# Kernel tuning notes

Hardware: AMD Instinct MI355X
Metric: run time of the kernel (lower is better)

Reference implementation:

```python
import jax, jax.numpy as jnp
import numpy as np

P = 30          # points per cloud (nr_points)
K = 20          # knn neighbors (k)
KS = 5          # spline kernel size (control points)
FN = 10         # filter_nr
EPS = 1e-8


def setup_inputs() -> dict:
    key = jax.random.key(0)
    ks = jax.random.split(key, 7)
    B = 16384
    pos = jax.random.normal(ks[0], (B * P, 3), dtype=jnp.float32)
    W = jax.random.normal(ks[1], (KS, FN), dtype=jnp.float32) * 0.5
    b_dsc = jnp.zeros((FN,), dtype=jnp.float32)
    w1 = jax.random.normal(ks[2], (FN, 256), dtype=jnp.float32) * (1.0 / np.sqrt(FN))
    b1 = jnp.zeros((256,), dtype=jnp.float32)
    w2 = jax.random.normal(ks[3], (256, 40), dtype=jnp.float32) * (1.0 / np.sqrt(256.0))
    b2 = jnp.zeros((40,), dtype=jnp.float32)
    return {"pos": pos, "W": W, "b_dsc": b_dsc, "w1": w1, "b1": b1, "w2": w2, "b2": b2}


def _dsc(pos, W, b_dsc):
    # pos: [N,3] -> per-point directional spline conv features [N, FN]
    B = pos.shape[0] // P
    p = pos.reshape(B, P, 3)
    # knn within each cloud (loop=False): pairwise sq dists, mask self
    d2 = jnp.sum((p[:, :, None, :] - p[:, None, :, :]) ** 2, axis=-1)  # [B,P,P]
    d2 = d2 + jnp.eye(P, dtype=d2.dtype) * 1e10
    _, idx = jax.lax.top_k(-d2, K)  # [B,P,K] nearest neighbor indices
    nb = jax.vmap(lambda pts, ii: pts[ii])(p, idx)  # [B,P,K,3] gather
    rel = nb - p[:, :, None, :]                      # [B,P,K,3]
    # normalize neighborhood into unit ball
    norm = jnp.sqrt(jnp.sum(rel * rel, axis=-1) + EPS)      # [B,P,K]
    scale = jnp.max(norm, axis=-1, keepdims=True) + EPS     # [B,P,1]
    rel_n = rel / scale[..., None]
    # dominant local direction via power iteration on 3x3 covariance
    C = jnp.einsum('bpki,bpkj->bpij', rel_n, rel_n)  # [B,P,3,3]
    v = jnp.ones((B, P, 3), dtype=pos.dtype) / jnp.sqrt(3.0)
    for _ in range(8):
        v = jnp.einsum('bpij,bpj->bpi', C, v)
        v = v / (jnp.sqrt(jnp.sum(v * v, axis=-1, keepdims=True)) + EPS)
    # directional coordinate in [-1,1] -> spline parameter in [0, KS-1]
    t = jnp.einsum('bpki,bpi->bpk', rel_n, v)        # [B,P,K]
    u = jnp.clip((t + 1.0) * 0.5, 0.0, 1.0) * (KS - 1)
    i0 = jnp.clip(jnp.floor(u), 0, KS - 2).astype(jnp.int32)  # [B,P,K]
    frac = (u - i0.astype(u.dtype))[..., None]                 # [B,P,K,1]
    feat = W[i0] * (1.0 - frac) + W[i0 + 1] * frac             # [B,P,K,FN]
    y = jnp.mean(feat, axis=2) + b_dsc                         # [B,P,FN]
    return y.reshape(B * P, FN)


def reference(pos, W, b_dsc, w1, b1, w2, b2):
    y = _dsc(pos, W, b_dsc)                  # [N, FN]
    y = jax.nn.sigmoid(y)
    ys = y.reshape(-1, P, FN).mean(axis=1)   # [B, FN]
    h = jax.nn.elu(ys @ w1 + b1)             # [B, 256]
    logits = h @ w2 + b2                     # [B, 40]
    return jax.nn.log_softmax(logits, axis=1)
```

## Files before the change

### kernel.cpp

```cpp
#include <hip/hip_runtime.h>
#include <math.h>

#define NP 30
#define KNN 20
#define KS 5
#define FN 10
#define EPS 1e-8f
#define CPB 8
#define T1 256

typedef __attribute__((ext_vector_type(8))) short short8v;
typedef __attribute__((ext_vector_type(4))) float float4v;

__device__ __forceinline__ float satf(float x) {
    return fminf(fmaxf(x, 0.0f), 1.0f);
}
__device__ __forceinline__ unsigned short bf16r(float f) {
    unsigned u = __float_as_uint(f);
    u += 0x7fffu + ((u >> 16) & 1u);
    return (unsigned short)(u >> 16);
}

#define PF(f) (((f) & 1) ? pp[(f) >> 1].y : pp[(f) >> 1].x)

__global__ __launch_bounds__(T1, 3) void fused_kernel(
    const float* __restrict__ pos,
    const float* __restrict__ W,
    const float* __restrict__ b_dsc,
    const float* __restrict__ w1,
    const float* __restrict__ b1,
    const float* __restrict__ w2,
    const float* __restrict__ b2,
    float* __restrict__ out,
    int B)
{
    __shared__ float sbuf[CPB * NP][FN + 1];
    __shared__ float wS[KS * FN];
    __shared__ float bS[FN];
    __shared__ float ysS[CPB][FN];
    __shared__ __align__(16) unsigned short hA[16][256];
    __shared__ float Lg[CPB][48];

    const int tid  = threadIdx.x;
    const int base = blockIdx.x * CPB;
    const int w    = tid >> 6;
    const int lane = tid & 63;

    if (tid < KS * FN) wS[tid] = W[tid];
    if (tid < FN)      bS[tid] = b_dsc[tid];
    __syncthreads();

    const int c = tid / NP;
    const int i = tid - c * NP;
    const bool active = (tid < CPB * NP) && (base + c < B);

    if (active) {
        const float* cb = pos + (size_t)(base + c) * (NP * 3);
        const float* ob = cb + i * 3;
        const float ox = ob[0], oy = ob[1], oz = ob[2];
        float2 pp[45];
        #pragma unroll
        for (int r = 0; r < 45; ++r) pp[r] = ((const float2*)cb)[r];

        float rx[NP], ry[NP], rz[NP];
        float vals[32];
        #pragma unroll
        for (int j = 0; j < NP; ++j) {
            float dx = PF(3*j+0) - ox;
            float dy = PF(3*j+1) - oy;
            float dz = PF(3*j+2) - oz;
            rx[j] = dx; ry[j] = dy; rz[j] = dz;
            vals[j] = fmaf(dz, dz, fmaf(dy, dy, dx * dx));
        }
        vals[30] = 1e11f;
        vals[31] = 1e11f;

        #pragma unroll
        for (int k = 2; k <= 16; k <<= 1) {
            #pragma unroll
            for (int jj = k >> 1; jj > 0; jj >>= 1) {
                #pragma unroll
                for (int tt = 0; tt < 32; ++tt) {
                    int l = tt ^ jj;
                    if (l > tt) {
                        float a  = vals[tt], b = vals[l];
                        float lo = fminf(a, b), hi = fmaxf(a, b);
                        if ((tt & k) == 0) { vals[tt] = lo; vals[l] = hi; }
                        else               { vals[tt] = hi; vals[l] = lo; }
                    }
                }
            }
        }
        #pragma unroll
        for (int q = 0; q < 16; ++q) vals[16+q] = fmaxf(vals[q], vals[16+q]);
        #pragma unroll
        for (int q = 0; q < 8; ++q)  vals[16+q] = fminf(vals[16+q], vals[24+q]);
        #pragma unroll
        for (int q = 0; q < 4; ++q)  vals[20+q] = fmaxf(vals[16+q], vals[20+q]);
        vals[20] = fminf(vals[20], vals[22]);
        vals[21] = fminf(vals[21], vals[23]);
        const float thr = fminf(vals[20], vals[21]);

        const float scale = sqrtf(thr + EPS) + EPS;
        const float inv_s = __builtin_amdgcn_rcpf(scale);

        float cxx=0.f, cxy=0.f, cxz=0.f, cyy=0.f, cyz=0.f, czz=0.f;
        #pragma unroll
        for (int j = 0; j < NP; ++j) {
            float dd = fmaf(rz[j], rz[j], fmaf(ry[j], ry[j], rx[j]*rx[j]));
            bool sel = (dd <= thr);
            float mx = sel ? rx[j] : 0.0f;
            float my = sel ? ry[j] : 0.0f;
            float mz = sel ? rz[j] : 0.0f;
            rx[j] = mx; ry[j] = my; rz[j] = mz;
            cxx = fmaf(mx, mx, cxx); cxy = fmaf(mx, my, cxy); cxz = fmaf(mx, mz, cxz);
            cyy = fmaf(my, my, cyy); cyz = fmaf(my, mz, cyz); czz = fmaf(mz, mz, czz);
        }

        float tr = cxx + cyy + czz + 1e-30f;
        float rt = __builtin_amdgcn_rcpf(tr);
        float xx = cxx*rt, xy = cxy*rt, xz = cxz*rt;
        float yy = cyy*rt, yz = cyz*rt, zz = czz*rt;
        #pragma unroll
        for (int it = 0; it < 3; ++it) {
            float nxx = fmaf(xx, xx, fmaf(xy, xy, xz * xz));
            float nxy = fmaf(xy, xx + yy, xz * yz);
            float nxz = fmaf(xz, xx + zz, xy * yz);
            float nyy = fmaf(xy, xy, fmaf(yy, yy, yz * yz));
            float nyz = fmaf(yz, yy + zz, xy * xz);
            float nzz = fmaf(xz, xz, fmaf(yz, yz, zz * zz));
            xx = nxx; xy = nxy; xz = nxz; yy = nyy; yz = nyz; zz = nzz;
        }
        float vx = xx + xy + xz;
        float vy = xy + yy + yz;
        float vz = xz + yz + zz;
        float nn = fmaf(vz, vz, fmaf(vy, vy, vx * vx)) + 1e-30f;
        float rr2 = __builtin_amdgcn_rsqf(nn) * inv_s * 2.0f;
        const float wax = vx * rr2, way = vy * rr2, waz = vz * rr2;

        float a0 = 0.f, a1 = 0.f, a3 = 0.f, s1 = 0.f;
        #pragma unroll
        for (int j = 0; j < NP; ++j) {
            float u = fmaf(rz[j], waz, fmaf(ry[j], way, fmaf(rx[j], wax, 2.0f)));
            a0 += satf(1.0f - fabsf(u));
            a1 += satf(1.0f - fabsf(u - 1.0f));
            a3 += satf(1.0f - fabsf(u - 3.0f));
            s1 += u;
        }
        const float P  = 30.0f - a0 - a1 - a3;
        const float Q  = s1 - a1 - 3.0f * a3;
        const float a4 = fmaf(0.5f, Q, -P);
        const float a2 = P - a4 - 10.0f;

        #pragma unroll
        for (int f = 0; f < FN; ++f) {
            float acc = fmaf(a0, wS[0*FN+f],
                        fmaf(a1, wS[1*FN+f],
                        fmaf(a2, wS[2*FN+f],
                        fmaf(a3, wS[3*FN+f],
                             a4 * wS[4*FN+f]))));
            float y = fmaf(acc, 1.0f / (float)KNN, bS[f]);
            sbuf[tid][f] = __builtin_amdgcn_rcpf(1.0f + __expf(-y));
        }
    }
    __syncthreads();

    if (tid < CPB * FN) {
        int c2 = tid / FN;
        int f  = tid - c2 * FN;
        float s = 0.0f;
        #pragma unroll
        for (int jj = 0; jj < NP; ++jj) s += sbuf[c2 * NP + jj][f];
        ysS[c2][f] = (base + c2 < B) ? s * (1.0f / (float)NP) : 0.0f;
    }
    {
        short8v z = {0, 0, 0, 0, 0, 0, 0, 0};
        *(short8v*)&hA[8 + (tid >> 5)][(tid & 31) * 8] = z;
    }
    __syncthreads();

    {
        float wv[FN];
        #pragma unroll
        for (int f = 0; f < FN; ++f) wv[f] = w1[f * 256 + tid];
        float bb = b1[tid];
        #pragma unroll
        for (int cc = 0; cc < CPB; ++cc) {
            float acc = bb;
            #pragma unroll
            for (int f = 0; f < FN; ++f) acc = fmaf(ysS[cc][f], wv[f], acc);
            float h = acc > 0.0f ? acc : __expf(acc) - 1.0f;
            hA[cc][tid] = bf16r(h);
        }
    }
    __syncthreads();

    if (w < 3) {
        const int  n   = w * 16 + (lane & 15);
        const bool nok = n < 40;
        const int  kg  = (lane >> 4) * 8;
        float4v acc = {0.f, 0.f, 0.f, 0.f};
        #pragma unroll
        for (int s = 0; s < 8; ++s) {
            short8v bfr;
            #pragma unroll
            for (int j = 0; j < 8; ++j) {
                float f = nok ? w2[(s * 32 + kg + j) * 40 + n] : 0.0f;
                bfr[j] = (short)bf16r(f);
            }
            short8v a = *(const short8v*)&hA[lane & 15][kg + s * 32];
            acc = __builtin_amdgcn_mfma_f32_16x16x32_bf16(a, bfr, acc, 0, 0, 0);
        }
        if (nok) {
            const float bc = b2[n];
            const int   r0 = (lane >> 4) * 4;
            #pragma unroll
            for (int r = 0; r < 4; ++r) {
                int rr = r0 + r;
                if (rr < CPB) Lg[rr][n] = acc[r] + bc;
            }
        }
    }
    __syncthreads();

    if (tid < CPB * 16) {
        int cl = tid >> 4, l = tid & 15;
        float v0 = Lg[cl][l];
        float v1 = Lg[cl][l + 16];
        float v2 = (l < 8) ? Lg[cl][l + 32] : -INFINITY;
        float m = fmaxf(fmaxf(v0, v1), v2);
        #pragma unroll
        for (int msk = 1; msk < 16; msk <<= 1) m = fmaxf(m, __shfl_xor(m, msk));
        float e = __expf(v0 - m) + __expf(v1 - m) + ((l < 8) ? __expf(v2 - m) : 0.0f);
        #pragma unroll
        for (int msk = 1; msk < 16; msk <<= 1) e += __shfl_xor(e, msk);
        float ls = m + __logf(e);
        int cloud = base + cl;
        if (cloud < B) {
            float* op = out + (size_t)cloud * 40;
            op[l]      = v0 - ls;
            op[16 + l] = v1 - ls;
            if (l < 8) op[32 + l] = v2 - ls;
        }
    }
}

extern "C" void kernel_launch(void* const* d_in, const int* in_sizes, int n_in,
                              void* d_out, int out_size, void* d_ws, size_t ws_size,
                              hipStream_t stream) {
    const float* pos   = (const float*)d_in[0];
    const float* W     = (const float*)d_in[1];
    const float* b_dsc = (const float*)d_in[2];
    const float* w1    = (const float*)d_in[3];
    const float* b1    = (const float*)d_in[4];
    const float* w2    = (const float*)d_in[5];
    const float* b2    = (const float*)d_in[6];

    const int N = in_sizes[0] / 3;
    const int B = N / NP;

    const int grid = (B + CPB - 1) / CPB;
    fused_kernel<<<grid, T1, 0, stream>>>(pos, W, b_dsc, w1, b1, w2, b2,
                                          (float*)d_out, B);
}
```

Measured before the change: 36.33 us.

## Stage cloud points in LDS and recompute offsets to cut registers

Loads each block's point clouds cooperatively into shared memory as float4. Each thread then recomputes relative offsets from LDS in every pass instead of holding 90 rx/ry/rz registers, and launch bounds rise from 3 to 6 blocks per SM to exploit the lower register pressure. It also XOR-swizzles the bf16 hA tile to reduce LDS bank conflicts in the MFMA operand loads. The trade-off is repeated LDS reads and ALU recomputation per point, plus a larger shared-memory footprint.

```diff
diff --git a/kernel.cpp b/kernel.cpp
--- a/kernel.cpp
+++ b/kernel.cpp
@@ -20,10 +20,11 @@
     u += 0x7fffu + ((u >> 16) & 1u);
     return (unsigned short)(u >> 16);
 }
-
-#define PF(f) (((f) & 1) ? pp[(f) >> 1].y : pp[(f) >> 1].x)
-
-__global__ __launch_bounds__(T1, 3) void fused_kernel(
+__device__ __forceinline__ int hA_idx(int row, int col ) {
+    return row * 256 + ((((col >> 3) ^ (row & 7)) << 3) | (col & 7));
+}
+
+__global__ __launch_bounds__(T1, 6) void fused_kernel(
     const float* __restrict__ pos,
     const float* __restrict__ W,
     const float* __restrict__ b_dsc,
@@ -34,11 +35,12 @@
     float* __restrict__ out,
     int B)
 {
+    __shared__ float4 ptsF[CPB * NP];
     __shared__ float sbuf[CPB * NP][FN + 1];
     __shared__ float wS[KS * FN];
     __shared__ float bS[FN];
     __shared__ float ysS[CPB][FN];
-    __shared__ __align__(16) unsigned short hA[16][256];
+    __shared__ __align__(16) unsigned short hA[16 * 256];
     __shared__ float Lg[CPB][48];
 
     const int tid  = threadIdx.x;
@@ -46,6 +48,14 @@
     const int w    = tid >> 6;
     const int lane = tid & 63;
 
+    {
+        const int lim = min(CPB * NP * 3, B * NP * 3 - base * NP * 3);
+        for (int d = tid; d < lim; d += T1) {
+            float v  = pos[(size_t)base * (NP * 3) + d];
+            int   pt = d / 3;
+            ((float*)&ptsF[pt])[d - pt * 3] = v;
+        }
+    }
     if (tid < KS * FN) wS[tid] = W[tid];
     if (tid < FN)      bS[tid] = b_dsc[tid];
     __syncthreads();
@@ -55,21 +65,15 @@
     const bool active = (tid < CPB * NP) && (base + c < B);
 
     if (active) {
-        const float* cb = pos + (size_t)(base + c) * (NP * 3);
-        const float* ob = cb + i * 3;
-        const float ox = ob[0], oy = ob[1], oz = ob[2];
-        float2 pp[45];
-        #pragma unroll
-        for (int r = 0; r < 45; ++r) pp[r] = ((const float2*)cb)[r];
-
-        float rx[NP], ry[NP], rz[NP];
+        const float4* cp = &ptsF[c * NP];
+        const float4 own = cp[i];
+        const float ox = own.x, oy = own.y, oz = own.z;
+
         float vals[32];
         #pragma unroll
         for (int j = 0; j < NP; ++j) {
-            float dx = PF(3*j+0) - ox;
-            float dy = PF(3*j+1) - oy;
-            float dz = PF(3*j+2) - oz;
-            rx[j] = dx; ry[j] = dy; rz[j] = dz;
+            float4 q = cp[j];
+            float dx = q.x - ox, dy = q.y - oy, dz = q.z - oz;
             vals[j] = fmaf(dz, dz, fmaf(dy, dy, dx * dx));
         }
         vals[30] = 1e11f;
@@ -104,15 +108,18 @@
         const float scale = sqrtf(thr + EPS) + EPS;
         const float inv_s = __builtin_amdgcn_rcpf(scale);
 
+        asm volatile("" ::: "memory");
+
         float cxx=0.f, cxy=0.f, cxz=0.f, cyy=0.f, cyz=0.f, czz=0.f;
         #pragma unroll
         for (int j = 0; j < NP; ++j) {
-            float dd = fmaf(rz[j], rz[j], fmaf(ry[j], ry[j], rx[j]*rx[j]));
+            float4 q = cp[j];
+            float dx = q.x - ox, dy = q.y - oy, dz = q.z - oz;
+            float dd = fmaf(dz, dz, fmaf(dy, dy, dx * dx));
             bool sel = (dd <= thr);
-            float mx = sel ? rx[j] : 0.0f;
-            float my = sel ? ry[j] : 0.0f;
-            float mz = sel ? rz[j] : 0.0f;
-            rx[j] = mx; ry[j] = my; rz[j] = mz;
+            float mx = sel ? dx : 0.0f;
+            float my = sel ? dy : 0.0f;
+            float mz = sel ? dz : 0.0f;
             cxx = fmaf(mx, mx, cxx); cxy = fmaf(mx, my, cxy); cxz = fmaf(mx, mz, cxz);
             cyy = fmaf(my, my, cyy); cyz = fmaf(my, mz, cyz); czz = fmaf(mz, mz, czz);
         }
@@ -138,10 +145,16 @@
         float rr2 = __builtin_amdgcn_rsqf(nn) * inv_s * 2.0f;
         const float wax = vx * rr2, way = vy * rr2, waz = vz * rr2;
 
+        asm volatile("" ::: "memory");
+
         float a0 = 0.f, a1 = 0.f, a3 = 0.f, s1 = 0.f;
         #pragma unroll
         for (int j = 0; j < NP; ++j) {
-            float u = fmaf(rz[j], waz, fmaf(ry[j], way, fmaf(rx[j], wax, 2.0f)));
+            float4 q = cp[j];
+            float dx = q.x - ox, dy = q.y - oy, dz = q.z - oz;
+            float dd = fmaf(dz, dz, fmaf(dy, dy, dx * dx));
+            float ur = fmaf(dz, waz, fmaf(dy, way, fmaf(dx, wax, 2.0f)));
+            float u  = (dd <= thr) ? ur : 2.0f;
             a0 += satf(1.0f - fabsf(u));
             a1 += satf(1.0f - fabsf(u - 1.0f));
             a3 += satf(1.0f - fabsf(u - 3.0f));
@@ -175,7 +188,7 @@
     }
     {
         short8v z = {0, 0, 0, 0, 0, 0, 0, 0};
-        *(short8v*)&hA[8 + (tid >> 5)][(tid & 31) * 8] = z;
+        *(short8v*)&hA[(8 + (tid >> 5)) * 256 + (tid & 31) * 8] = z;
     }
     __syncthreads();
 
@@ -190,7 +203,7 @@
             #pragma unroll
             for (int f = 0; f < FN; ++f) acc = fmaf(ysS[cc][f], wv[f], acc);
             float h = acc > 0.0f ? acc : __expf(acc) - 1.0f;
-            hA[cc][tid] = bf16r(h);
+            hA[hA_idx(cc, tid)] = bf16r(h);
         }
     }
     __syncthreads();
@@ -208,7 +221,7 @@
                 float f = nok ? w2[(s * 32 + kg + j) * 40 + n] : 0.0f;
                 bfr[j] = (short)bf16r(f);
             }
-            short8v a = *(const short8v*)&hA[lane & 15][kg + s * 32];
+            short8v a = *(const short8v*)&hA[hA_idx(lane & 15, kg + s * 32)];
             acc = __builtin_amdgcn_mfma_f32_16x16x32_bf16(a, bfr, acc, 0, 0, 0);
         }
         if (nok) {
```

Measured after the change: 36.12 us. No clear change (-0.6%).
